# Kernel tuning notes

Hardware: AMD Instinct MI355X
Metric: run time of the kernel (lower is better)

## Reference

```python
import jax, jax.numpy as jnp
import numpy as np

BATCH, NUM_HEADS, SEQ, HEAD_DIM = 2, 32, 2048, 128
QMAX = 127.0  # symmetric int8 quantization range


def _fake_quant(x):
    # per-(head, token) symmetric int8 quantization + dequantization
    scale = jnp.max(jnp.abs(x), axis=-1, keepdims=True) / QMAX
    scale = jnp.maximum(scale, jnp.asarray(1e-8, x.dtype))
    q = jnp.clip(jnp.round(x / scale), -QMAX, QMAX)  # packed int8 values
    return q * scale  # dequantized


def setup_inputs() -> dict:
    key = jax.random.key(0)
    kq, kk, kv = jax.random.split(key, 3)
    shape = (BATCH, NUM_HEADS, SEQ, HEAD_DIM)
    return {
        "query": jax.random.normal(kq, shape, dtype=jnp.float32),
        "key": jax.random.normal(kk, shape, dtype=jnp.float32),
        "value": jax.random.normal(kv, shape, dtype=jnp.float32),
    }


def reference(query, key, value):
    # quantize K/V on the fly into the cache, then attend over dequantized K/V
    k_dq = _fake_quant(key)
    v_dq = _fake_quant(value)
    scale = jnp.asarray(1.0 / np.sqrt(HEAD_DIM), query.dtype)
    logits = jnp.einsum("bhqd,bhkd->bhqk", query, k_dq) * scale  # [B,H,Sq,Sk]
    weights = jax.nn.softmax(logits, axis=-1)
    out = jnp.einsum("bhqk,bhkd->bhqd", weights, v_dq)
    return out
```

## Files before the change

### kernel.cpp

```cpp
#include <hip/hip_runtime.h>
#include <hip/hip_bf16.h>

#define B 2
#define H 32
#define S 2048
#define D 128
#define NT 32

typedef __bf16 bf16x8 __attribute__((ext_vector_type(8)));
typedef float f32x4 __attribute__((ext_vector_type(4)));

union BF8U { unsigned int u[4]; unsigned short s[8]; bf16x8 b; int4 i4; };

static constexpr float INV_SQRT_D = 0.08838834764831845f;
static constexpr float LOG2E = 1.4426950408889634f;
static constexpr int NROWS = B * H * S;

__device__ __forceinline__ unsigned short bfbits(float f) {
    union { __bf16 h; unsigned short s; } cv;
    cv.h = (__bf16)f;
    return cv.s;
}
__device__ __forceinline__ unsigned int pack2bf(float a, float b) {
    union { unsigned short s[2]; unsigned int u; } cv;
    cv.s[0] = bfbits(a); cv.s[1] = bfbits(b);
    return cv.u;
}

typedef unsigned int u32;
__device__ __forceinline__ void async_ld16(const unsigned short* g, unsigned short* l) {
    __builtin_amdgcn_global_load_lds(
        (const __attribute__((address_space(1))) u32*)g,
        (__attribute__((address_space(3))) u32*)l, 16, 0, 0);
}

__global__ __launch_bounds__(256) void quant_k_kernel(
    const float* __restrict__ x, unsigned short* __restrict__ kpk,
    float* __restrict__ scl)
{
    const int row  = blockIdx.x * 4 + (threadIdx.x >> 6);
    const int lane = threadIdx.x & 63;
    const float2 v = *(const float2*)(x + (size_t)row * D + lane * 2);
    float m = fmaxf(fabsf(v.x), fabsf(v.y));
    #pragma unroll
    for (int off = 32; off; off >>= 1) m = fmaxf(m, __shfl_xor(m, off));
    const float scale = fmaxf(m / 127.0f, 1e-8f);
    const float q0 = fminf(fmaxf(rintf(v.x / scale), -127.0f), 127.0f);
    const float q1 = fminf(fmaxf(rintf(v.y / scale), -127.0f), 127.0f);
    const int bh = row >> 11, kv = row & 2047;
    const int t = kv >> 6, r = kv & 63, s = lane >> 2;
    unsigned short* dst = kpk + ((((size_t)bh * NT + t) * 16 + s) * 64 + r) * 8 + (lane & 3) * 2;
    *(unsigned int*)dst = pack2bf(q0, q1);
    if (lane == 0) scl[row] = scale * INV_SQRT_D * LOG2E;
}

__global__ __launch_bounds__(256) void quant_v_kernel(
    const float* __restrict__ x, unsigned short* __restrict__ vpk)
{
    __shared__ __align__(16) unsigned short vt[D][72];
    const int bh = blockIdx.y;
    const int t  = blockIdx.x;
    const int s0 = t * 64;
    const int tid = threadIdx.x;
    const int wave = tid >> 6, lane = tid & 63;

    #pragma unroll 1
    for (int i = 0; i < 16; i++) {
        const int tok = wave * 16 + i;
        const float2 v = *(const float2*)(x + ((size_t)bh * S + s0 + tok) * D + lane * 2);
        float m = fmaxf(fabsf(v.x), fabsf(v.y));
        #pragma unroll
        for (int off = 32; off; off >>= 1) m = fmaxf(m, __shfl_xor(m, off));
        const float scale = fmaxf(m / 127.0f, 1e-8f);
        const float q0 = fminf(fmaxf(rintf(v.x / scale), -127.0f), 127.0f);
        const float q1 = fminf(fmaxf(rintf(v.y / scale), -127.0f), 127.0f);
        vt[lane * 2    ][tok] = bfbits(q0 * scale);
        vt[lane * 2 + 1][tok] = bfbits(q1 * scale);
    }
    __syncthreads();
    const int d = tid & 127, sh = tid >> 7;
    const size_t tb = ((size_t)bh * NT + t) * 8192;
    #pragma unroll
    for (int p = 0; p < 4; p++) {
        const int s = p * 2 + sh, kk = s >> 2, gg = s & 3;
        BF8U o;
        *(unsigned long long*)&o.s[0] = *(const unsigned long long*)&vt[d][32 * kk + 4 * gg];
        *(unsigned long long*)&o.s[4] = *(const unsigned long long*)&vt[d][32 * kk + 16 + 4 * gg];
        *(int4*)(vpk + tb + ((size_t)s * 128 + d) * 8) = o.i4;
    }
}

__global__ __launch_bounds__(256, 2) void attn_kernel(
    const float* __restrict__ Q, const unsigned short* __restrict__ Kpk,
    const float* __restrict__ Ksc, const unsigned short* __restrict__ Vpk,
    float* __restrict__ Out)
{
    __shared__ __align__(16) unsigned short Kb[2][8192];

    const int wg = blockIdx.x;
    const int swz = (wg & 7) * 128 + (wg >> 3);
    const int bh = swz >> 4;
    const int qt = swz & 15;
    const int tid = threadIdx.x;
    const int wave = tid >> 6, lane = tid & 63;
    const int g = lane >> 4, c = lane & 15;

    const size_t tbase = (size_t)bh * NT * 8192;
    const size_t scb   = (size_t)bh * S;

    auto STAGE = [&](int tn, int pb) {
        const unsigned short* kt = Kpk + tbase + (size_t)tn * 8192;
        #pragma unroll
        for (int i = 0; i < 4; i++) {
            const int ch = wave * 4 + i;
            async_ld16(kt + ch * 512 + lane * 8, &Kb[pb][ch * 512]);
        }
    };

    bf16x8 qfA[4], qfB[4];
    {
        const float* qpA = Q + ((size_t)bh * S + qt * 128 + wave * 32 + c) * D + g * 8;
        const float* qpB = qpA + 16 * D;
        #pragma unroll
        for (int kk = 0; kk < 4; kk++) {
            float4 a = *(const float4*)(qpA + kk * 32);
            float4 b = *(const float4*)(qpA + kk * 32 + 4);
            BF8U t8;
            t8.s[0] = bfbits(a.x); t8.s[1] = bfbits(a.y); t8.s[2] = bfbits(a.z); t8.s[3] = bfbits(a.w);
            t8.s[4] = bfbits(b.x); t8.s[5] = bfbits(b.y); t8.s[6] = bfbits(b.z); t8.s[7] = bfbits(b.w);
            qfA[kk] = t8.b;
            a = *(const float4*)(qpB + kk * 32);
            b = *(const float4*)(qpB + kk * 32 + 4);
            t8.s[0] = bfbits(a.x); t8.s[1] = bfbits(a.y); t8.s[2] = bfbits(a.z); t8.s[3] = bfbits(a.w);
            t8.s[4] = bfbits(b.x); t8.s[5] = bfbits(b.y); t8.s[6] = bfbits(b.z); t8.s[7] = bfbits(b.w);
            qfB[kk] = t8.b;
        }
    }

    f32x4 accA[8], accB[8];
    const f32x4 zero = {0.f, 0.f, 0.f, 0.f};
    #pragma unroll
    for (int i = 0; i < 8; i++) { accA[i] = zero; accB[i] = zero; }
    float mA = -1e30f, lA = 0.f, mB = -1e30f, lB = 0.f;

    STAGE(0, 0);
    __syncthreads();

    #pragma unroll 1
    for (int t = 0; t < NT; t++) {
        const int cur = t & 1;
        if (t + 1 < NT) STAGE(t + 1, cur ^ 1);

        f32x4 sA[4], sB[4];
        __builtin_amdgcn_s_setprio(1);
        #pragma unroll
        for (int n = 0; n < 4; n++) {
            sA[n] = zero; sB[n] = zero;
            #pragma unroll
            for (int kk = 0; kk < 4; kk++) {
                bf16x8 kf = *(const bf16x8*)&Kb[cur][((4 * kk + g) * 64 + n * 16 + c) * 8];
                sA[n] = __builtin_amdgcn_mfma_f32_16x16x32_bf16(kf, qfA[kk], sA[n], 0, 0, 0);
                sB[n] = __builtin_amdgcn_mfma_f32_16x16x32_bf16(kf, qfB[kk], sB[n], 0, 0, 0);
            }
        }
        __builtin_amdgcn_s_setprio(0);

        const unsigned short* vtg = Vpk + tbase + (size_t)t * 8192;
        bf16x8 vf[2][8];
        #pragma unroll
        for (int kk = 0; kk < 2; kk++)
            #pragma unroll
            for (int nd = 0; nd < 8; nd++)
                vf[kk][nd] = *(const bf16x8*)(vtg + ((kk * 4 + g) * 128 + nd * 16 + c) * 8);

        const float* kscp = Ksc + scb + t * 64;
        float mxA = -1e30f, mxB = -1e30f;
        #pragma unroll
        for (int n = 0; n < 4; n++) {
            const f32x4 ks4 = *(const f32x4*)(kscp + n * 16 + 4 * g);
            #pragma unroll
            for (int j = 0; j < 4; j++) {
                sA[n][j] *= ks4[j];
                sB[n][j] *= ks4[j];
                mxA = fmaxf(mxA, sA[n][j]);
                mxB = fmaxf(mxB, sB[n][j]);
            }
        }
        mxA = fmaxf(mxA, __shfl_xor(mxA, 16));
        mxA = fmaxf(mxA, __shfl_xor(mxA, 32));
        mxB = fmaxf(mxB, __shfl_xor(mxB, 16));
        mxB = fmaxf(mxB, __shfl_xor(mxB, 32));

        if (!__all(mxA - mA <= 8.0f)) {
            const float mnew = fmaxf(mA, mxA);
            const float corr = exp2f(mA - mnew);
            mA = mnew; lA *= corr;
            float cq[4];
            #pragma unroll
            for (int r = 0; r < 4; r++) cq[r] = __shfl(corr, 4 * g + r);
            #pragma unroll
            for (int nd = 0; nd < 8; nd++)
                #pragma unroll
                for (int r = 0; r < 4; r++) accA[nd][r] *= cq[r];
        }
        if (!__all(mxB - mB <= 8.0f)) {
            const float mnew = fmaxf(mB, mxB);
            const float corr = exp2f(mB - mnew);
            mB = mnew; lB *= corr;
            float cq[4];
            #pragma unroll
            for (int r = 0; r < 4; r++) cq[r] = __shfl(corr, 4 * g + r);
            #pragma unroll
            for (int nd = 0; nd < 8; nd++)
                #pragma unroll
                for (int r = 0; r < 4; r++) accB[nd][r] *= cq[r];
        }

        float psA = 0.f, psB = 0.f;
        #pragma unroll
        for (int n = 0; n < 4; n++) {
            #pragma unroll
            for (int j = 0; j < 4; j++) {
                float p = exp2f(sA[n][j] - mA);
                psA += p;
                sA[n][j] = p;
                p = exp2f(sB[n][j] - mB);
                psB += p;
                sB[n][j] = p;
            }
        }
        psA += __shfl_xor(psA, 16);
        psA += __shfl_xor(psA, 32);
        lA += psA;
        psB += __shfl_xor(psB, 16);
        psB += __shfl_xor(psB, 32);
        lB += psB;

        __builtin_amdgcn_s_setprio(1);
        #pragma unroll
        for (int kk = 0; kk < 2; kk++) {
            BF8U a8, b8;
            a8.u[0] = pack2bf(sA[2 * kk][0], sA[2 * kk][1]);
            a8.u[1] = pack2bf(sA[2 * kk][2], sA[2 * kk][3]);
            a8.u[2] = pack2bf(sA[2 * kk + 1][0], sA[2 * kk + 1][1]);
            a8.u[3] = pack2bf(sA[2 * kk + 1][2], sA[2 * kk + 1][3]);
            b8.u[0] = pack2bf(sB[2 * kk][0], sB[2 * kk][1]);
            b8.u[1] = pack2bf(sB[2 * kk][2], sB[2 * kk][3]);
            b8.u[2] = pack2bf(sB[2 * kk + 1][0], sB[2 * kk + 1][1]);
            b8.u[3] = pack2bf(sB[2 * kk + 1][2], sB[2 * kk + 1][3]);
            const bf16x8 pfA = a8.b, pfB = b8.b;
            #pragma unroll
            for (int nd = 0; nd < 8; nd++) {
                accA[nd] = __builtin_amdgcn_mfma_f32_16x16x32_bf16(pfA, vf[kk][nd], accA[nd], 0, 0, 0);
                accB[nd] = __builtin_amdgcn_mfma_f32_16x16x32_bf16(pfB, vf[kk][nd], accB[nd], 0, 0, 0);
            }
        }
        __builtin_amdgcn_s_setprio(0);

        __syncthreads();
    }

    const float invA = 1.0f / lA, invB = 1.0f / lB;
    float iqA[4], iqB[4];
    #pragma unroll
    for (int r = 0; r < 4; r++) {
        iqA[r] = __shfl(invA, 4 * g + r);
        iqB[r] = __shfl(invB, 4 * g + r);
    }
    const size_t obase = ((size_t)bh * S + qt * 128 + wave * 32) * (size_t)D;
    #pragma unroll
    for (int r = 0; r < 4; r++) {
        const int q = 4 * g + r;
        #pragma unroll
        for (int nd = 0; nd < 8; nd++) {
            Out[obase + (size_t)q * D + nd * 16 + c] = accA[nd][r] * iqA[r];
            Out[obase + (size_t)(q + 16) * D + nd * 16 + c] = accB[nd][r] * iqB[r];
        }
    }
}

extern "C" void kernel_launch(void* const* d_in, const int* in_sizes, int n_in,
                              void* d_out, int out_size, void* d_ws, size_t ws_size,
                              hipStream_t stream) {
    const float* q = (const float*)d_in[0];
    const float* k = (const float*)d_in[1];
    const float* v = (const float*)d_in[2];
    float* out = (float*)d_out;

    const size_t ELEMS = (size_t)NROWS * D;
    unsigned short* kpk = (unsigned short*)d_ws;
    unsigned short* vpk = kpk + ELEMS;
    float* ks = (float*)(vpk + ELEMS);

    quant_k_kernel<<<NROWS / 4, 256, 0, stream>>>(k, kpk, ks);
    quant_v_kernel<<<dim3(NT, B * H), 256, 0, stream>>>(v, vpk);
    attn_kernel<<<1024, 256, 0, stream>>>(q, kpk, ks, vpk, out);
}
```

Before: 285.5 us.

## Split V fragment loads and raise occupancy target to three waves per SIMD

Splits the per-tile V register fragments into two halves: the second half is loaded from global memory only after the first half's PV MFMAs, which lowers peak VGPR use. Raises launch bounds from 2 to 3 blocks per CU. Replaces exp2f with raw v_exp_f32 inline asm to drop range-handling code. The tradeoff is a more exposed global-load latency for the second V half, and possible spills under the tighter register budget.

```diff
diff --git a/kernel.cpp b/kernel.cpp
--- a/kernel.cpp
+++ b/kernel.cpp
@@ -25,6 +25,11 @@
     union { unsigned short s[2]; unsigned int u; } cv;
     cv.s[0] = bfbits(a); cv.s[1] = bfbits(b);
     return cv.u;
+}
+__device__ __forceinline__ float exp2_raw(float x) {
+    float r;
+    asm("v_exp_f32 %0, %1" : "=v"(r) : "v"(x));
+    return r;
 }
 
 typedef unsigned int u32;
@@ -90,7 +95,7 @@
     }
 }
 
-__global__ __launch_bounds__(256, 2) void attn_kernel(
+__global__ __launch_bounds__(256, 3) void attn_kernel(
     const float* __restrict__ Q, const unsigned short* __restrict__ Kpk,
     const float* __restrict__ Ksc, const unsigned short* __restrict__ Vpk,
     float* __restrict__ Out)
@@ -166,12 +171,10 @@
         __builtin_amdgcn_s_setprio(0);
 
         const unsigned short* vtg = Vpk + tbase + (size_t)t * 8192;
-        bf16x8 vf[2][8];
-        #pragma unroll
-        for (int kk = 0; kk < 2; kk++)
-            #pragma unroll
-            for (int nd = 0; nd < 8; nd++)
-                vf[kk][nd] = *(const bf16x8*)(vtg + ((kk * 4 + g) * 128 + nd * 16 + c) * 8);
+        bf16x8 vf0[8];
+        #pragma unroll
+        for (int nd = 0; nd < 8; nd++)
+            vf0[nd] = *(const bf16x8*)(vtg + ((0 * 4 + g) * 128 + nd * 16 + c) * 8);
 
         const float* kscp = Ksc + scb + t * 64;
         float mxA = -1e30f, mxB = -1e30f;
@@ -193,7 +196,7 @@
 
         if (!__all(mxA - mA <= 8.0f)) {
             const float mnew = fmaxf(mA, mxA);
-            const float corr = exp2f(mA - mnew);
+            const float corr = exp2_raw(mA - mnew);
             mA = mnew; lA *= corr;
             float cq[4];
             #pragma unroll
@@ -205,7 +208,7 @@
         }
         if (!__all(mxB - mB <= 8.0f)) {
             const float mnew = fmaxf(mB, mxB);
-            const float corr = exp2f(mB - mnew);
+            const float corr = exp2_raw(mB - mnew);
             mB = mnew; lB *= corr;
             float cq[4];
             #pragma unroll
@@ -221,10 +224,10 @@
         for (int n = 0; n < 4; n++) {
             #pragma unroll
             for (int j = 0; j < 4; j++) {
-                float p = exp2f(sA[n][j] - mA);
+                float p = exp2_raw(sA[n][j] - mA);
                 psA += p;
                 sA[n][j] = p;
-                p = exp2f(sB[n][j] - mB);
+                p = exp2_raw(sB[n][j] - mB);
                 psB += p;
                 sB[n][j] = p;
             }
@@ -236,24 +239,42 @@
         psB += __shfl_xor(psB, 32);
         lB += psB;
 
+        BF8U a80, b80, a81, b81;
+        a80.u[0] = pack2bf(sA[0][0], sA[0][1]);
+        a80.u[1] = pack2bf(sA[0][2], sA[0][3]);
+        a80.u[2] = pack2bf(sA[1][0], sA[1][1]);
+        a80.u[3] = pack2bf(sA[1][2], sA[1][3]);
+        b80.u[0] = pack2bf(sB[0][0], sB[0][1]);
+        b80.u[1] = pack2bf(sB[0][2], sB[0][3]);
+        b80.u[2] = pack2bf(sB[1][0], sB[1][1]);
+        b80.u[3] = pack2bf(sB[1][2], sB[1][3]);
+        a81.u[0] = pack2bf(sA[2][0], sA[2][1]);
+        a81.u[1] = pack2bf(sA[2][2], sA[2][3]);
+        a81.u[2] = pack2bf(sA[3][0], sA[3][1]);
+        a81.u[3] = pack2bf(sA[3][2], sA[3][3]);
+        b81.u[0] = pack2bf(sB[2][0], sB[2][1]);
+        b81.u[1] = pack2bf(sB[2][2], sB[2][3]);
+        b81.u[2] = pack2bf(sB[3][0], sB[3][1]);
+        b81.u[3] = pack2bf(sB[3][2], sB[3][3]);
+
         __builtin_amdgcn_s_setprio(1);
         #pragma unroll
-        for (int kk = 0; kk < 2; kk++) {
-            BF8U a8, b8;
-            a8.u[0] = pack2bf(sA[2 * kk][0], sA[2 * kk][1]);
-            a8.u[1] = pack2bf(sA[2 * kk][2], sA[2 * kk][3]);
-            a8.u[2] = pack2bf(sA[2 * kk + 1][0], sA[2 * kk + 1][1]);
-            a8.u[3] = pack2bf(sA[2 * kk + 1][2], sA[2 * kk + 1][3]);
-            b8.u[0] = pack2bf(sB[2 * kk][0], sB[2 * kk][1]);
-            b8.u[1] = pack2bf(sB[2 * kk][2], sB[2 * kk][3]);
-            b8.u[2] = pack2bf(sB[2 * kk + 1][0], sB[2 * kk + 1][1]);
-            b8.u[3] = pack2bf(sB[2 * kk + 1][2], sB[2 * kk + 1][3]);
-            const bf16x8 pfA = a8.b, pfB = b8.b;
-            #pragma unroll
-            for (int nd = 0; nd < 8; nd++) {
-                accA[nd] = __builtin_amdgcn_mfma_f32_16x16x32_bf16(pfA, vf[kk][nd], accA[nd], 0, 0, 0);
-                accB[nd] = __builtin_amdgcn_mfma_f32_16x16x32_bf16(pfB, vf[kk][nd], accB[nd], 0, 0, 0);
-            }
+        for (int nd = 0; nd < 8; nd++) {
+            accA[nd] = __builtin_amdgcn_mfma_f32_16x16x32_bf16(a80.b, vf0[nd], accA[nd], 0, 0, 0);
+            accB[nd] = __builtin_amdgcn_mfma_f32_16x16x32_bf16(b80.b, vf0[nd], accB[nd], 0, 0, 0);
+        }
+        __builtin_amdgcn_s_setprio(0);
+
+        bf16x8 vf1[8];
+        #pragma unroll
+        for (int nd = 0; nd < 8; nd++)
+            vf1[nd] = *(const bf16x8*)(vtg + ((1 * 4 + g) * 128 + nd * 16 + c) * 8);
+
+        __builtin_amdgcn_s_setprio(1);
+        #pragma unroll
+        for (int nd = 0; nd < 8; nd++) {
+            accA[nd] = __builtin_amdgcn_mfma_f32_16x16x32_bf16(a81.b, vf1[nd], accA[nd], 0, 0, 0);
+            accB[nd] = __builtin_amdgcn_mfma_f32_16x16x32_bf16(b81.b, vf1[nd], accB[nd], 0, 0, 0);
         }
         __builtin_amdgcn_s_setprio(0);
 
```

Result: slower. 333.8 us (+16.9%).
